# Kernel optimization log

Measured on AMD Instinct MI355X. Metric: run time of the kernel, lower is better.

## Reference

```python
import jax, jax.numpy as jnp
import numpy as np


def setup_inputs() -> dict:
    key = jax.random.key(0)
    k1, k2, k3 = jax.random.split(key, 3)
    B, H, W, D, C, F = 2, 96, 128, 64, 32, 32
    images = jax.random.normal(k1, (B, H, W, D, C), dtype=jnp.float32)
    base_plane = jax.random.randint(k2, (B, H, W, 1), 0, 16, dtype=jnp.int32)
    kernel = jax.random.normal(k3, (3, 3, 3, C, F), dtype=jnp.float32) * 0.05
    default_value = jnp.zeros((), dtype=jnp.float32)
    return {"images": images, "base_plane": base_plane,
            "kernel": kernel, "default_value": default_value}


def _sparse_conv3d(images, base_plane, kernel, default_value):
    # images: [B,H,W,D,C] stored depth band per pixel, starting at base_plane
    # base_plane: [B,H,W,1] int, kernel: [KH,KW,KD,C,F]
    B, H, W, D, C = images.shape
    KH, KW, KD, _, F = kernel.shape
    ph, pw, pd = KH // 2, KW // 2, KD // 2
    bp = base_plane[..., 0]  # [B,H,W]

    # pad spatially once; out-of-image neighbors read default_value
    img_pad = jnp.pad(images, ((0, 0), (ph, ph), (pw, pw), (0, 0), (0, 0)))
    bp_pad = jnp.pad(bp, ((0, 0), (ph, ph), (pw, pw)))
    sp_valid_pad = jnp.pad(jnp.ones((H, W), dtype=bool),
                           ((ph, ph), (pw, pw)))

    d_grid = jnp.arange(D)[None, None, None, :]  # [1,1,1,D]
    out = jnp.zeros((B, H, W, D, F), dtype=images.dtype)

    for kh in range(KH):
        for kw in range(KW):
            img_s = img_pad[:, kh:kh + H, kw:kw + W]          # [B,H,W,D,C]
            bp_s = bp_pad[:, kh:kh + H, kw:kw + W]            # [B,H,W]
            sp_valid = sp_valid_pad[kh:kh + H, kw:kw + W]     # [H,W]
            for kd in range(KD):
                # neighbor stored-depth index = (d + bp) + (kd-pd) - bp_neighbor
                idx = d_grid + (bp - bp_s)[:, :, :, None] + (kd - pd)  # [B,H,W,D]
                valid = (idx >= 0) & (idx < D) & sp_valid[None, :, :, None]
                g = jnp.take_along_axis(
                    img_s, jnp.clip(idx, 0, D - 1)[..., None], axis=3)
                val = jnp.where(valid[..., None], g, default_value)
                out = out + jnp.einsum('bhwdc,cf->bhwdf', val,
                                       kernel[kh, kw, kd])
    return out


def reference(images, base_plane, kernel, default_value):
    return _sparse_conv3d(images, base_plane, kernel, default_value)
```

## Files before the change

### kernel.cpp

```cpp
#include <hip/hip_runtime.h>
#include <hip/hip_bf16.h>

#define Bn 2
#define Hn 96
#define Wn 128
#define Dn 64
#define Cn 32
#define Fn 32
#define TH 2
#define TW 8
#define CH (TH + 2)
#define CW (TW + 2)
#define NCOLS (CH * CW)

typedef short bf16x8 __attribute__((ext_vector_type(8)));
typedef float f32x4  __attribute__((ext_vector_type(4)));

__device__ __forceinline__ ushort f2bf(float x) {
    __hip_bfloat16 h = __float2bfloat16(x);
    return *reinterpret_cast<ushort*>(&h);
}

__device__ __forceinline__ int swz_off(int r, int slot) {
    return r * 32 + ((slot ^ ((r >> 1) & 3)) << 3);
}

__global__ void prep_kT(const float* __restrict__ kern, ushort* __restrict__ kT) {
    const int e = blockIdx.x * 256 + threadIdx.x;
    if (e >= 27 * Cn * Fn) return;
    const int c  = e & 31;
    const int f  = (e >> 5) & 31;
    const int kk = e >> 10;
    kT[e] = f2bf(kern[kk * (Cn * Fn) + c * Fn + f]);
}

__global__ __launch_bounds__(1024, 4) void sconv3d_mfma(
    const float*  __restrict__ img,
    const int*    __restrict__ bp,
    const float*  __restrict__ kern,
    const ushort* __restrict__ kT,
    const float*  __restrict__ dvp,
    float*        __restrict__ out)
{
    __shared__ ushort colS[NCOLS * Dn * Cn];

    const int blk = blockIdx.x;
    const int wt  = blk % (Wn / TW);
    const int ht  = (blk / (Wn / TW)) % (Hn / TH);
    const int b   = blk / ((Wn / TW) * (Hn / TH));
    const int h0  = ht * TH;
    const int w0  = wt * TW;

    const int tid  = threadIdx.x;
    const int lane = tid & 63;
    const int wave = tid >> 6;
    const int ph   = wave >> 3;
    const int pw   = wave & 7;
    const int h    = h0 + ph;
    const int w    = w0 + pw;

    const int lrow = lane & 15;
    const int lgrp = lane >> 4;

    const float dv  = *dvp;
    const int   bpc = bp[(b * Hn + h) * Wn + w];

    int  sh[9];
    bool tv[9];
#pragma unroll
    for (int kh = 0; kh < 3; ++kh)
#pragma unroll
        for (int kw = 0; kw < 3; ++kw) {
            const int hh = h - 1 + kh;
            const int ww = w - 1 + kw;
            const bool v = (hh >= 0) && (hh < Hn) && (ww >= 0) && (ww < Wn);
            tv[kh * 3 + kw] = v;
            sh[kh * 3 + kw] = v ? (bpc - bp[(b * Hn + hh) * Wn + ww]) : 0;
        }

    for (int it = 0; it < NCOLS * 512 / 1024; ++it) {
        const int e  = it * 1024 + tid;
        const int j  = e >> 9;
        const int sl = e & 511;
        const int hh = h0 - 1 + j / CW;
        const int ww = w0 - 1 + j % CW;
        if (hh < 0 || hh >= Hn || ww < 0 || ww >= Wn) continue;
        const float4 v = *(const float4*)(img +
            (size_t)((b * Hn + hh) * Wn + ww) * (Dn * Cn) + sl * 4);
        ushort4 u;
        u.x = f2bf(v.x); u.y = f2bf(v.y); u.z = f2bf(v.z); u.w = f2bf(v.w);
        *(ushort4*)&colS[j * (Dn * Cn) + swz_off(sl >> 3, (sl >> 1) & 3) + (sl & 1) * 4] = u;
    }
    __syncthreads();

    f32x4 acc[4][2];
#pragma unroll
    for (int i = 0; i < 4; ++i)
#pragma unroll
        for (int j = 0; j < 2; ++j) acc[i][j] = (f32x4)0.f;

#pragma unroll
    for (int kh = 0; kh < 3; ++kh) {
#pragma unroll
        for (int kw = 0; kw < 3; ++kw) {
            if (!tv[kh * 3 + kw]) continue;
            const int s = sh[kh * 3 + kw];
            const ushort* colp = &colS[((ph + kh) * CW + (pw + kw)) * (Dn * Cn)];
#pragma unroll
            for (int kd = 0; kd < 3; ++kd) {
                const int kk = (kh * 3 + kw) * 3 + kd;
                const bf16x8 bf0 = *(const bf16x8*)&kT[(kk * Fn + lrow)      * Cn + lgrp * 8];
                const bf16x8 bf1 = *(const bf16x8*)&kT[(kk * Fn + lrow + 16) * Cn + lgrp * 8];
                const int X = s + kd - 1;
                __builtin_amdgcn_s_setprio(1);
#pragma unroll
                for (int dt = 0; dt < 4; ++dt) {
                    const int  idx   = dt * 16 + lrow + X;
                    const int  ci    = idx < 0 ? 0 : (idx > 63 ? 63 : idx);
                    const bool valid = (idx == ci);
                    bf16x8 af = *(const bf16x8*)&colp[swz_off(ci, lgrp)];
                    if (!valid) af = (bf16x8)0;
                    acc[dt][0] = __builtin_amdgcn_mfma_f32_16x16x32_bf16(af, bf0, acc[dt][0], 0, 0, 0);
                    acc[dt][1] = __builtin_amdgcn_mfma_f32_16x16x32_bf16(af, bf1, acc[dt][1], 0, 0, 0);
                }
                __builtin_amdgcn_s_setprio(0);
            }
        }
    }

    if (dv != 0.0f) {
#pragma unroll
        for (int kh = 0; kh < 3; ++kh)
#pragma unroll
            for (int kw = 0; kw < 3; ++kw) {
                const bool sp = tv[kh * 3 + kw];
                const int  s  = sh[kh * 3 + kw];
                for (int kd = 0; kd < 3; ++kd) {
                    float ks0 = 0.f, ks1 = 0.f;
                    for (int c = 0; c < Cn; ++c) {
                        const float* kp = kern + (size_t)(((kh * 3 + kw) * 3 + kd) * Cn + c) * Fn;
                        ks0 += kp[lrow];
                        ks1 += kp[16 + lrow];
                    }
                    for (int dt = 0; dt < 4; ++dt)
                        for (int j = 0; j < 4; ++j) {
                            const int d   = dt * 16 + lgrp * 4 + j;
                            const int idx = d + s + kd - 1;
                            const bool valid = sp && (idx >= 0) && (idx < Dn);
                            if (!valid) { acc[dt][0][j] += dv * ks0; acc[dt][1][j] += dv * ks1; }
                        }
                }
            }
    }

    const size_t pixbase = ((size_t)(b * Hn + h) * Wn + w) * (Dn * Fn);
#pragma unroll
    for (int dt = 0; dt < 4; ++dt)
#pragma unroll
        for (int ft = 0; ft < 2; ++ft)
#pragma unroll
            for (int j = 0; j < 4; ++j) {
                const int d = dt * 16 + lgrp * 4 + j;
                const int f = ft * 16 + lrow;
                out[pixbase + d * Fn + f] = acc[dt][ft][j];
            }
}

extern "C" void kernel_launch(void* const* d_in, const int* in_sizes, int n_in,
                              void* d_out, int out_size, void* d_ws, size_t ws_size,
                              hipStream_t stream) {
    const float* img  = (const float*)d_in[0];
    const int*   bp   = (const int*)d_in[1];
    const float* kern = (const float*)d_in[2];
    const float* dvp  = (const float*)d_in[3];
    float* out = (float*)d_out;
    ushort* kT = (ushort*)d_ws;

    hipLaunchKernelGGL(prep_kT, dim3(108), dim3(256), 0, stream, kern, kT);

    const int nblk = Bn * (Hn / TH) * (Wn / TW);
    hipLaunchKernelGGL(sconv3d_mfma, dim3(nblk), dim3(1024), 0, stream,
                       img, bp, kern, kT, dvp, out);
}
```

Measured before the change: 184.8 us.

## Split halo staging into two phases overlapping loads with first-row compute

Image staging now happens in two halves. The top two halo rows are loaded and written to shared memory first. The bottom two rows are prefetched into registers and written to LDS after the first barrier. Compute for kh=0 then runs before a second barrier, so part of the global load latency overlaps MFMA work. The inner loop is also restructured: kernel fragments for all kd are preloaded, and the A-fragment addresses are derived from one swizzled offset with validity checks only at the edge tiles. This raises register pressure (ten float4 prefetch registers plus six B fragments) at launch bounds of 1024 threads, and it depends on the shift s being bounded so that the middle tiles stay in range.

```diff
diff --git a/kernel.cpp b/kernel.cpp
--- a/kernel.cpp
+++ b/kernel.cpp
@@ -9,9 +9,8 @@
 #define Fn 32
 #define TH 2
 #define TW 8
-#define CH (TH + 2)
 #define CW (TW + 2)
-#define NCOLS (CH * CW)
+#define NCOLS (4 * CW)
 
 typedef short bf16x8 __attribute__((ext_vector_type(8)));
 typedef float f32x4  __attribute__((ext_vector_type(4)));
@@ -78,20 +77,50 @@
             sh[kh * 3 + kw] = v ? (bpc - bp[(b * Hn + hh) * Wn + ww]) : 0;
         }
 
-    for (int it = 0; it < NCOLS * 512 / 1024; ++it) {
+
+    float4 pv[10];
+#pragma unroll
+    for (int it = 0; it < 10; ++it) {
         const int e  = it * 1024 + tid;
-        const int j  = e >> 9;
+        const int jl = e >> 9;
         const int sl = e & 511;
-        const int hh = h0 - 1 + j / CW;
-        const int ww = w0 - 1 + j % CW;
-        if (hh < 0 || hh >= Hn || ww < 0 || ww >= Wn) continue;
-        const float4 v = *(const float4*)(img +
-            (size_t)((b * Hn + hh) * Wn + ww) * (Dn * Cn) + sl * 4);
+        const int hh = h0 + 1 + (jl >= CW ? 1 : 0);
+        const int ww = w0 - 1 + (jl % CW);
+        const bool v = (hh < Hn) && (ww >= 0) && (ww < Wn);
+        pv[it] = v ? *(const float4*)(img +
+                      (size_t)((b * Hn + hh) * Wn + ww) * (Dn * Cn) + sl * 4)
+                   : make_float4(0.f, 0.f, 0.f, 0.f);
+    }
+
+#pragma unroll
+    for (int it = 0; it < 10; ++it) {
+        const int e  = it * 1024 + tid;
+        const int jl = e >> 9;
+        const int sl = e & 511;
+        const int hh = h0 - 1 + (jl >= CW ? 1 : 0);
+        const int ww = w0 - 1 + (jl % CW);
+        if (hh >= 0 && ww >= 0 && ww < Wn) {
+            const float4 v = *(const float4*)(img +
+                (size_t)((b * Hn + hh) * Wn + ww) * (Dn * Cn) + sl * 4);
+            ushort4 u;
+            u.x = f2bf(v.x); u.y = f2bf(v.y); u.z = f2bf(v.z); u.w = f2bf(v.w);
+            *(ushort4*)&colS[jl * (Dn * Cn)
+                             + swz_off(sl >> 3, (sl >> 1) & 3) + (sl & 1) * 4] = u;
+        }
+    }
+    __syncthreads();
+
+#pragma unroll
+    for (int it = 0; it < 10; ++it) {
+        const int e  = it * 1024 + tid;
+        const int jl = e >> 9;
+        const int sl = e & 511;
         ushort4 u;
-        u.x = f2bf(v.x); u.y = f2bf(v.y); u.z = f2bf(v.z); u.w = f2bf(v.w);
-        *(ushort4*)&colS[j * (Dn * Cn) + swz_off(sl >> 3, (sl >> 1) & 3) + (sl & 1) * 4] = u;
-    }
-    __syncthreads();
+        u.x = f2bf(pv[it].x); u.y = f2bf(pv[it].y);
+        u.z = f2bf(pv[it].z); u.w = f2bf(pv[it].w);
+        *(ushort4*)&colS[(20 + jl) * (Dn * Cn)
+                         + swz_off(sl >> 3, (sl >> 1) & 3) + (sl & 1) * 4] = u;
+    }
 
     f32x4 acc[4][2];
 #pragma unroll
@@ -99,34 +128,53 @@
 #pragma unroll
         for (int j = 0; j < 2; ++j) acc[i][j] = (f32x4)0.f;
 
-#pragma unroll
-    for (int kh = 0; kh < 3; ++kh) {
+    auto compute_kh = [&](int kh) {
 #pragma unroll
         for (int kw = 0; kw < 3; ++kw) {
             if (!tv[kh * 3 + kw]) continue;
             const int s = sh[kh * 3 + kw];
             const ushort* colp = &colS[((ph + kh) * CW + (pw + kw)) * (Dn * Cn)];
+            const int kkb = (kh * 3 + kw) * 3;
+            bf16x8 bfr[3][2];
 #pragma unroll
             for (int kd = 0; kd < 3; ++kd) {
-                const int kk = (kh * 3 + kw) * 3 + kd;
-                const bf16x8 bf0 = *(const bf16x8*)&kT[(kk * Fn + lrow)      * Cn + lgrp * 8];
-                const bf16x8 bf1 = *(const bf16x8*)&kT[(kk * Fn + lrow + 16) * Cn + lgrp * 8];
-                const int X = s + kd - 1;
-                __builtin_amdgcn_s_setprio(1);
-#pragma unroll
-                for (int dt = 0; dt < 4; ++dt) {
-                    const int  idx   = dt * 16 + lrow + X;
-                    const int  ci    = idx < 0 ? 0 : (idx > 63 ? 63 : idx);
-                    const bool valid = (idx == ci);
-                    bf16x8 af = *(const bf16x8*)&colp[swz_off(ci, lgrp)];
-                    if (!valid) af = (bf16x8)0;
-                    acc[dt][0] = __builtin_amdgcn_mfma_f32_16x16x32_bf16(af, bf0, acc[dt][0], 0, 0, 0);
-                    acc[dt][1] = __builtin_amdgcn_mfma_f32_16x16x32_bf16(af, bf1, acc[dt][1], 0, 0, 0);
+                bfr[kd][0] = *(const bf16x8*)&kT[((kkb + kd) * Fn + lrow)      * Cn + lgrp * 8];
+                bfr[kd][1] = *(const bf16x8*)&kT[((kkb + kd) * Fn + lrow + 16) * Cn + lgrp * 8];
+            }
+            __builtin_amdgcn_s_setprio(1);
+#pragma unroll
+            for (int kd = 0; kd < 3; ++kd) {
+                const int i1 = 16 + lrow + s + kd - 1;
+                const int o1 = swz_off(i1, lgrp);
+                const bf16x8 a1 = *(const bf16x8*)&colp[o1];
+                acc[1][0] = __builtin_amdgcn_mfma_f32_16x16x32_bf16(a1, bfr[kd][0], acc[1][0], 0, 0, 0);
+                acc[1][1] = __builtin_amdgcn_mfma_f32_16x16x32_bf16(a1, bfr[kd][1], acc[1][1], 0, 0, 0);
+                const bf16x8 a2 = *(const bf16x8*)&colp[o1 + 512];
+                acc[2][0] = __builtin_amdgcn_mfma_f32_16x16x32_bf16(a2, bfr[kd][0], acc[2][0], 0, 0, 0);
+                acc[2][1] = __builtin_amdgcn_mfma_f32_16x16x32_bf16(a2, bfr[kd][1], acc[2][1], 0, 0, 0);
+                {
+                    const bool v = (i1 >= 16);
+                    bf16x8 a0 = *(const bf16x8*)&colp[v ? o1 - 512 : o1];
+                    if (!v) a0 = (bf16x8)0;
+                    acc[0][0] = __builtin_amdgcn_mfma_f32_16x16x32_bf16(a0, bfr[kd][0], acc[0][0], 0, 0, 0);
+                    acc[0][1] = __builtin_amdgcn_mfma_f32_16x16x32_bf16(a0, bfr[kd][1], acc[0][1], 0, 0, 0);
                 }
-                __builtin_amdgcn_s_setprio(0);
-            }
+                {
+                    const bool v = (i1 <= 31);
+                    bf16x8 a3 = *(const bf16x8*)&colp[v ? o1 + 1024 : o1];
+                    if (!v) a3 = (bf16x8)0;
+                    acc[3][0] = __builtin_amdgcn_mfma_f32_16x16x32_bf16(a3, bfr[kd][0], acc[3][0], 0, 0, 0);
+                    acc[3][1] = __builtin_amdgcn_mfma_f32_16x16x32_bf16(a3, bfr[kd][1], acc[3][1], 0, 0, 0);
+                }
+            }
+            __builtin_amdgcn_s_setprio(0);
         }
-    }
+    };
+
+    compute_kh(0);
+    __syncthreads();
+    compute_kh(1);
+    compute_kh(2);
 
     if (dv != 0.0f) {
 #pragma unroll
```

New measurement: 197.1 us. +6.6%, slower.
